# Performance work log

Hardware: AMD Instinct MI355X
Metric: run time of the kernel (lower is better)

Reference implementation:

```python
import jax, jax.numpy as jnp
import numpy as np

N_NODES = 100000
NFEAT, NHID, NCLASS = 128, 64, 40
N_EDGES = 1600000


def setup_inputs() -> dict:
    key = jax.random.key(0)
    k1, k2, k3, k4, k5, k6 = jax.random.split(key, 6)
    x = jax.random.normal(k1, (N_NODES, NFEAT), dtype=jnp.float32)
    edge_index = jax.random.randint(k2, (2, N_EDGES), 0, N_NODES, dtype=jnp.int64)
    s1 = 1.0 / np.sqrt(NFEAT)
    s2 = 1.0 / np.sqrt(NHID)
    W1 = jax.random.uniform(k3, (NFEAT, NHID), jnp.float32, -s1, s1)
    b1 = jax.random.uniform(k4, (NHID,), jnp.float32, -s1, s1)
    W2 = jax.random.uniform(k5, (NHID, NCLASS), jnp.float32, -s2, s2)
    b2 = jax.random.uniform(k6, (NCLASS,), jnp.float32, -s2, s2)
    return {"x": x, "edge_index": edge_index, "W1": W1, "b1": b1, "W2": W2, "b2": b2}


def _gcn_conv(x, W, b, src, dst, n_nodes):
    # linear
    h = x @ W + b  # [N, out]
    # degree of source nodes (self-loops already included in src/dst)
    deg = jax.ops.segment_sum(jnp.ones_like(src, dtype=h.dtype), src, num_segments=n_nodes)
    dinv = deg ** -0.5  # deg >= 1 due to self-loops
    norm = dinv[src] * dinv[dst]  # [E]
    msg = norm[:, None] * h[src]  # gather + normalize, [E, out]
    return jax.ops.segment_sum(msg, dst, num_segments=n_nodes)  # scatter-add


def reference(x, edge_index, W1, b1, W2, b2):
    n = x.shape[0]
    loop = jnp.arange(n, dtype=edge_index.dtype)
    src = jnp.concatenate([edge_index[0], loop])
    dst = jnp.concatenate([edge_index[1], loop])
    h = _gcn_conv(x, W1, b1, src, dst, n)
    h = jax.nn.relu(h)
    # dropout is identity in eval mode
    h = _gcn_conv(h, W2, b2, src, dst, n)
    return jax.nn.log_softmax(h, axis=1)
```

## Files before the change

### kernel.cpp

```cpp
#include <hip/hip_runtime.h>
#include <math.h>

#define NFEAT 128
#define NHID 64
#define NCLASS 40
#define NCHUNK 64
#define RANGE 16384

typedef _Float16 half4_t __attribute__((ext_vector_type(4)));
typedef _Float16 half8_t __attribute__((ext_vector_type(8)));
typedef float f32x4 __attribute__((ext_vector_type(4)));

__global__ __launch_bounds__(1024) void histdeg_kernel(
    const int* __restrict__ src, const int* __restrict__ dst, int E, int n,
    int nrange, unsigned short* __restrict__ deg_p,
    unsigned short* __restrict__ hist_p) {
    __shared__ unsigned int degc[RANGE / 2];
    __shared__ unsigned int histc[RANGE / 2];
    int c = blockIdx.x / nrange;
    int r = blockIdx.x - c * nrange;
    int r0 = r * RANGE;
    for (int i = threadIdx.x; i < RANGE / 2; i += 1024) {
        degc[i] = 0u;
        histc[i] = 0u;
    }
    __syncthreads();
    int e0 = (int)((long long)E * c / NCHUNK);
    int e1 = (int)((long long)E * (c + 1) / NCHUNK);
    for (int e = e0 + threadIdx.x * 4; e + 4 <= e1; e += 4096) {
        int4 s4 = *(const int4*)(src + e);
        int4 d4 = *(const int4*)(dst + e);
        int ss[4] = {s4.x, s4.y, s4.z, s4.w};
        int dd[4] = {d4.x, d4.y, d4.z, d4.w};
#pragma unroll
        for (int k = 0; k < 4; ++k) {
            int s = ss[k] - r0, d = dd[k] - r0;
            if ((unsigned)s < (unsigned)RANGE)
                atomicAdd(&degc[s >> 1], 1u << ((s & 1) * 16));
            if ((unsigned)d < (unsigned)RANGE)
                atomicAdd(&histc[d >> 1], 1u << ((d & 1) * 16));
        }
    }
    int tb = e0 + ((e1 - e0) & ~3);
    for (int e = tb + threadIdx.x; e < e1; e += 1024) {
        int s = src[e] - r0, d = dst[e] - r0;
        if ((unsigned)s < (unsigned)RANGE)
            atomicAdd(&degc[s >> 1], 1u << ((s & 1) * 16));
        if ((unsigned)d < (unsigned)RANGE)
            atomicAdd(&histc[d >> 1], 1u << ((d & 1) * 16));
    }
    __syncthreads();
    int hi = n - r0; if (hi > RANGE) hi = RANGE;
    for (int i = threadIdx.x; i < hi; i += 1024) {
        unsigned dv = (degc[i >> 1] >> ((i & 1) * 16)) & 0xFFFFu;
        unsigned hv = (histc[i >> 1] >> ((i & 1) * 16)) & 0xFFFFu;
        deg_p[(size_t)c * n + r0 + i] = (unsigned short)dv;
        hist_p[(size_t)c * n + r0 + i] = (unsigned short)hv;
    }
}

__global__ void reduce_kernel(const unsigned short* __restrict__ deg_p,
                              const unsigned short* __restrict__ hist_p,
                              float* __restrict__ dinv,
                              int* __restrict__ htot, int n) {
    int i = blockIdx.x * blockDim.x + threadIdx.x;
    if (i >= n) return;
    int d = 1, h = 0;
#pragma unroll 8
    for (int c = 0; c < NCHUNK; ++c) {
        d += deg_p[(size_t)c * n + i];
        h += hist_p[(size_t)c * n + i];
    }
    dinv[i] = rsqrtf((float)d);
    htot[i] = h;
}

__global__ void scan_block_kernel(const int* __restrict__ hist,
                                  int* __restrict__ scanned,
                                  int* __restrict__ bsums, int n) {
    __shared__ int tmp[256];
    int i = blockIdx.x * 256 + threadIdx.x;
    int v = (i < n) ? hist[i] : 0;
    tmp[threadIdx.x] = v;
    __syncthreads();
#pragma unroll
    for (int off = 1; off < 256; off <<= 1) {
        int t = (threadIdx.x >= off) ? tmp[threadIdx.x - off] : 0;
        __syncthreads();
        tmp[threadIdx.x] += t;
        __syncthreads();
    }
    if (i < n) scanned[i] = tmp[threadIdx.x] - v;
    if (threadIdx.x == 255) bsums[blockIdx.x] = tmp[255];
}

__global__ void scan_partials_kernel(int* __restrict__ bsums, int nb) {
    __shared__ int tmp[512];
    int v = (threadIdx.x < nb) ? bsums[threadIdx.x] : 0;
    tmp[threadIdx.x] = v;
    __syncthreads();
#pragma unroll
    for (int off = 1; off < 512; off <<= 1) {
        int t = (threadIdx.x >= off) ? tmp[threadIdx.x - off] : 0;
        __syncthreads();
        tmp[threadIdx.x] += t;
        __syncthreads();
    }
    if (threadIdx.x < nb) bsums[threadIdx.x] = tmp[threadIdx.x] - v;
}

__global__ void scan_add_kernel(const int* __restrict__ scanned,
                                const int* __restrict__ bsums,
                                int* __restrict__ row_start, int n, int E) {
    int i = blockIdx.x * 256 + threadIdx.x;
    if (i < n) row_start[i] = scanned[i] + bsums[blockIdx.x];
    if (i == 0) row_start[n] = E;
}

__global__ void base_kernel(const int* __restrict__ row_start,
                            const unsigned short* __restrict__ hist_p,
                            int* __restrict__ bases, int n) {
    int i = blockIdx.x * blockDim.x + threadIdx.x;
    if (i >= n) return;
    int r = row_start[i];
#pragma unroll 8
    for (int c = 0; c < NCHUNK; ++c) {
        bases[(size_t)c * n + i] = r;
        r += hist_p[(size_t)c * n + i];
    }
}

__global__ __launch_bounds__(1024) void scatter_kernel(
    const int* __restrict__ src, const int* __restrict__ dst, int E, int n,
    int nrange, const int* __restrict__ bases, int* __restrict__ es) {
    __shared__ int cur[RANGE];
    int c = blockIdx.x / nrange;
    int r = blockIdx.x - c * nrange;
    int r0 = r * RANGE;
    int hi = n - r0; if (hi > RANGE) hi = RANGE;
    for (int i = threadIdx.x; i < hi; i += 1024)
        cur[i] = bases[(size_t)c * n + r0 + i];
    __syncthreads();
    int e0 = (int)((long long)E * c / NCHUNK);
    int e1 = (int)((long long)E * (c + 1) / NCHUNK);
    for (int e = e0 + threadIdx.x * 4; e + 4 <= e1; e += 4096) {
        int4 s4 = *(const int4*)(src + e);
        int4 d4 = *(const int4*)(dst + e);
        int ss[4] = {s4.x, s4.y, s4.z, s4.w};
        int dd[4] = {d4.x, d4.y, d4.z, d4.w};
#pragma unroll
        for (int k = 0; k < 4; ++k) {
            int d = dd[k] - r0;
            if ((unsigned)d < (unsigned)hi) {
                int pos = atomicAdd(&cur[d], 1);
                es[pos] = ss[k];
            }
        }
    }
    int tb = e0 + ((e1 - e0) & ~3);
    for (int e = tb + threadIdx.x; e < e1; e += 1024) {
        int d = dst[e] - r0;
        if ((unsigned)d < (unsigned)hi) {
            int pos = atomicAdd(&cur[d], 1);
            es[pos] = src[e];
        }
    }
}

__global__ __launch_bounds__(256) void gemm1_mfma_kernel(
    const float* __restrict__ x, const float* __restrict__ W1,
    const float* __restrict__ b1, const float* __restrict__ dinv,
    _Float16* __restrict__ H1, int n) {
    int wave = threadIdx.x >> 6;
    int lane = threadIdx.x & 63;
    int lr = lane & 15;
    int kg = lane >> 4;
    half8_t bf[4][4];
    float b1v[4];
#pragma unroll
    for (int t = 0; t < 4; ++t) {
        int col = t * 16 + lr;
        b1v[t] = b1[col];
#pragma unroll
        for (int ks = 0; ks < 4; ++ks) {
            int kb = ks * 32 + kg * 8;
            half8_t hb;
#pragma unroll
            for (int j = 0; j < 8; ++j) hb[j] = (_Float16)W1[(kb + j) * NHID + col];
            bf[ks][t] = hb;
        }
    }
    int nt16 = (n + 15) >> 4;
    for (int gt = blockIdx.x * 4 + wave; gt < nt16; gt += gridDim.x * 4) {
        int m0 = gt * 16;
        int arow = m0 + lr; if (arow >= n) arow = n - 1;
        f32x4 acc[4] = {f32x4{0,0,0,0}, f32x4{0,0,0,0}, f32x4{0,0,0,0}, f32x4{0,0,0,0}};
#pragma unroll
        for (int ks = 0; ks < 4; ++ks) {
            const float* ap = x + (size_t)arow * NFEAT + ks * 32 + kg * 8;
            float4 a0 = *(const float4*)ap;
            float4 a1 = *(const float4*)(ap + 4);
            half8_t af;
            af[0] = (_Float16)a0.x; af[1] = (_Float16)a0.y;
            af[2] = (_Float16)a0.z; af[3] = (_Float16)a0.w;
            af[4] = (_Float16)a1.x; af[5] = (_Float16)a1.y;
            af[6] = (_Float16)a1.z; af[7] = (_Float16)a1.w;
#pragma unroll
            for (int t = 0; t < 4; ++t)
                acc[t] = __builtin_amdgcn_mfma_f32_16x16x32_f16(af, bf[ks][t], acc[t], 0, 0, 0);
        }
        int r0 = m0 + kg * 4;
        float dv[4];
#pragma unroll
        for (int r = 0; r < 4; ++r) {
            int rr = r0 + r;
            dv[r] = (rr < n) ? dinv[rr] : 0.f;
        }
#pragma unroll
        for (int t = 0; t < 4; ++t)
#pragma unroll
            for (int r = 0; r < 4; ++r) {
                int rr = r0 + r;
                if (rr < n)
                    H1[(size_t)rr * NHID + t * 16 + lr] =
                        (_Float16)((acc[t][r] + b1v[t]) * dv[r]);
            }
    }
}

__global__ __launch_bounds__(256) void agg1_kernel(
    const int* __restrict__ es, const int* __restrict__ row_start,
    const float* __restrict__ dinv, const _Float16* __restrict__ H1,
    _Float16* __restrict__ AGG, int n) {
    int wave = threadIdx.x >> 6;
    int lane = threadIdx.x & 63;
    int q = lane >> 4;
    int m = lane & 15;
    int stride = gridDim.x * 4;
    for (int node = blockIdx.x * 4 + wave; node < n; node += stride) {
        int e0 = row_start[node], e1 = row_start[node + 1];
        float a0 = 0.f, a1 = 0.f, a2 = 0.f, a3 = 0.f;
        for (int e = e0; e < e1; e += 64) {
            int cnt = e1 - e; if (cnt > 64) cnt = 64;
            int myE = es[e + ((lane < cnt) ? lane : 0)];
            for (int j = 0; j < cnt; j += 16) {
#pragma unroll
                for (int p = 0; p < 4; ++p) {
                    int jj = j + 4 * p + q;
                    int rr = __shfl(myE, jj, 64);
                    if (jj < cnt) {
                        half4_t v = *(const half4_t*)(H1 + (size_t)rr * NHID + 4 * m);
                        a0 += (float)v[0]; a1 += (float)v[1];
                        a2 += (float)v[2]; a3 += (float)v[3];
                    }
                }
            }
        }
        if (q == 0) {
            half4_t v = *(const half4_t*)(H1 + (size_t)node * NHID + 4 * m);
            a0 += (float)v[0]; a1 += (float)v[1];
            a2 += (float)v[2]; a3 += (float)v[3];
        }
        a0 += __shfl_xor(a0, 16, 64); a0 += __shfl_xor(a0, 32, 64);
        a1 += __shfl_xor(a1, 16, 64); a1 += __shfl_xor(a1, 32, 64);
        a2 += __shfl_xor(a2, 16, 64); a2 += __shfl_xor(a2, 32, 64);
        a3 += __shfl_xor(a3, 16, 64); a3 += __shfl_xor(a3, 32, 64);
        float di = dinv[node];
        if (lane < 16) {
            half4_t o;
            o[0] = (_Float16)fmaxf(a0 * di, 0.f);
            o[1] = (_Float16)fmaxf(a1 * di, 0.f);
            o[2] = (_Float16)fmaxf(a2 * di, 0.f);
            o[3] = (_Float16)fmaxf(a3 * di, 0.f);
            *(half4_t*)(AGG + (size_t)node * NHID + 4 * lane) = o;
        }
    }
}

__global__ __launch_bounds__(256) void gemm2_mfma_kernel(
    const _Float16* __restrict__ AGG, const float* __restrict__ W2,
    const float* __restrict__ b2, const float* __restrict__ dinv,
    _Float16* __restrict__ H2, int n) {
    int wave = threadIdx.x >> 6;
    int lane = threadIdx.x & 63;
    int lr = lane & 15;
    int kg = lane >> 4;
    half8_t bf[2][3];
    float b2v[3];
#pragma unroll
    for (int t = 0; t < 3; ++t) {
        int col = t * 16 + lr;
        b2v[t] = (col < NCLASS) ? b2[col] : 0.f;
#pragma unroll
        for (int ks = 0; ks < 2; ++ks) {
            int kb = ks * 32 + kg * 8;
            half8_t hb;
#pragma unroll
            for (int j = 0; j < 8; ++j)
                hb[j] = (col < NCLASS) ? (_Float16)W2[(kb + j) * NCLASS + col]
                                       : (_Float16)0.f;
            bf[ks][t] = hb;
        }
    }
    int nt16 = (n + 15) >> 4;
    for (int gt = blockIdx.x * 4 + wave; gt < nt16; gt += gridDim.x * 4) {
        int m0 = gt * 16;
        int arow = m0 + lr; if (arow >= n) arow = n - 1;
        f32x4 acc[3] = {f32x4{0,0,0,0}, f32x4{0,0,0,0}, f32x4{0,0,0,0}};
#pragma unroll
        for (int ks = 0; ks < 2; ++ks) {
            half8_t af = *(const half8_t*)(AGG + (size_t)arow * NHID + ks * 32 + kg * 8);
#pragma unroll
            for (int t = 0; t < 3; ++t)
                acc[t] = __builtin_amdgcn_mfma_f32_16x16x32_f16(af, bf[ks][t], acc[t], 0, 0, 0);
        }
        int r0 = m0 + kg * 4;
        float dv[4];
#pragma unroll
        for (int r = 0; r < 4; ++r) {
            int rr = r0 + r;
            dv[r] = (rr < n) ? dinv[rr] : 0.f;
        }
#pragma unroll
        for (int t = 0; t < 3; ++t) {
            int col = t * 16 + lr;
#pragma unroll
            for (int r = 0; r < 4; ++r) {
                int rr = r0 + r;
                if (rr < n)
                    H2[(size_t)rr * 64 + col] =
                        (col < NCLASS) ? (_Float16)((acc[t][r] + b2v[t]) * dv[r])
                                       : (_Float16)0.f;
            }
        }
    }
}

__global__ __launch_bounds__(256) void agg2_lsm_kernel(
    const int* __restrict__ es, const int* __restrict__ row_start,
    const float* __restrict__ dinv, const _Float16* __restrict__ H2,
    float* __restrict__ out, int n) {
    int wave = threadIdx.x >> 6;
    int lane = threadIdx.x & 63;
    int q = lane >> 4;
    int m = lane & 15;
    int stride = gridDim.x * 4;
    for (int node = blockIdx.x * 4 + wave; node < n; node += stride) {
        int e0 = row_start[node], e1 = row_start[node + 1];
        float a0 = 0.f, a1 = 0.f, a2 = 0.f, a3 = 0.f;
        for (int e = e0; e < e1; e += 64) {
            int cnt = e1 - e; if (cnt > 64) cnt = 64;
            int myE = es[e + ((lane < cnt) ? lane : 0)];
            for (int j = 0; j < cnt; j += 16) {
#pragma unroll
                for (int p = 0; p < 4; ++p) {
                    int jj = j + 4 * p + q;
                    int rr = __shfl(myE, jj, 64);
                    if (jj < cnt) {
                        half4_t v = *(const half4_t*)(H2 + (size_t)rr * 64 + 4 * m);
                        a0 += (float)v[0]; a1 += (float)v[1];
                        a2 += (float)v[2]; a3 += (float)v[3];
                    }
                }
            }
        }
        if (q == 0) {
            half4_t v = *(const half4_t*)(H2 + (size_t)node * 64 + 4 * m);
            a0 += (float)v[0]; a1 += (float)v[1];
            a2 += (float)v[2]; a3 += (float)v[3];
        }
        a0 += __shfl_xor(a0, 16, 64); a0 += __shfl_xor(a0, 32, 64);
        a1 += __shfl_xor(a1, 16, 64); a1 += __shfl_xor(a1, 32, 64);
        a2 += __shfl_xor(a2, 16, 64); a2 += __shfl_xor(a2, 32, 64);
        a3 += __shfl_xor(a3, 16, 64); a3 += __shfl_xor(a3, 32, 64);
        float di = dinv[node];
        float v0 = a0 * di, v1 = a1 * di, v2 = a2 * di, v3 = a3 * di;
        bool valid = (m < 10);
        float vmax = valid ? fmaxf(fmaxf(v0, v1), fmaxf(v2, v3)) : -INFINITY;
#pragma unroll
        for (int off = 8; off; off >>= 1) vmax = fmaxf(vmax, __shfl_xor(vmax, off, 64));
        float sume = valid ? (__expf(v0 - vmax) + __expf(v1 - vmax) +
                              __expf(v2 - vmax) + __expf(v3 - vmax)) : 0.f;
#pragma unroll
        for (int off = 8; off; off >>= 1) sume += __shfl_xor(sume, off, 64);
        float lse = __logf(sume) + vmax;
        if (lane < 10) {
            float4 o = make_float4(v0 - lse, v1 - lse, v2 - lse, v3 - lse);
            *(float4*)(out + (size_t)node * NCLASS + 4 * lane) = o;
        }
    }
}

extern "C" void kernel_launch(void* const* d_in, const int* in_sizes, int n_in,
                              void* d_out, int out_size, void* d_ws, size_t ws_size,
                              hipStream_t stream) {
    const float* x  = (const float*)d_in[0];
    const int*   ei = (const int*)d_in[1];
    const float* W1 = (const float*)d_in[2];
    const float* b1 = (const float*)d_in[3];
    const float* W2 = (const float*)d_in[4];
    const float* b2 = (const float*)d_in[5];
    float* out = (float*)d_out;

    const int n = in_sizes[0] / NFEAT;
    const int E = in_sizes[1] / 2;
    const int* src = ei;
    const int* dst = ei + E;
    const int nrange = (n + RANGE - 1) / RANGE;

    char* ws = (char*)d_ws;
    float*          dinv      = (float*)(ws + 0);
    int*            htot      = (int*)(ws + (512 << 10));
    int*            scanned   = (int*)(ws + (1024 << 10));
    int*            row_start = (int*)(ws + (1536 << 10));
    int*            bsums     = (int*)(ws + (2048 << 10));
    unsigned short* deg_p     = (unsigned short*)(ws + (3u << 20));
    unsigned short* hist_p    = (unsigned short*)(ws + (16u << 20));
    int*            bases     = (int*)(ws + (29u << 20));
    int*            es        = (int*)(ws + (3u << 20));
    _Float16*       H2        = (_Float16*)(ws + (16u << 20));
    _Float16*       H1        = (_Float16*)(ws + (29u << 20));
    _Float16*       AGG       = (_Float16*)(ws + (42u << 20));

    const int blk = 256;
    const int nblk_n = (n + blk - 1) / blk;
    const int gridbin = NCHUNK * nrange;

    histdeg_kernel<<<gridbin, 1024, 0, stream>>>(src, dst, E, n, nrange, deg_p, hist_p);
    reduce_kernel<<<nblk_n, blk, 0, stream>>>(deg_p, hist_p, dinv, htot, n);

    scan_block_kernel<<<nblk_n, blk, 0, stream>>>(htot, scanned, bsums, n);
    scan_partials_kernel<<<1, 512, 0, stream>>>(bsums, nblk_n);
    scan_add_kernel<<<nblk_n, blk, 0, stream>>>(scanned, bsums, row_start, n, E);
    base_kernel<<<nblk_n, blk, 0, stream>>>(row_start, hist_p, bases, n);

    scatter_kernel<<<gridbin, 1024, 0, stream>>>(src, dst, E, n, nrange, bases, es);

    gemm1_mfma_kernel<<<512, blk, 0, stream>>>(x, W1, b1, dinv, H1, n);

    agg1_kernel<<<4096, blk, 0, stream>>>(es, row_start, dinv, H1, AGG, n);

    gemm2_mfma_kernel<<<512, blk, 0, stream>>>(AGG, W2, b2, dinv, H2, n);

    agg2_lsm_kernel<<<4096, blk, 0, stream>>>(es, row_start, dinv, H2, out, n);
}
```

Before: 309.9 us.

## Widen histogram range, compact H2 to 40 columns, use 32-bit index math

The histogram kernel now covers 32768 nodes per block, which halves the number of passes over the edge list. The scatter kernel keeps its 16384-node range. H2 is now stored with a 40-column stride instead of a padded 64, and agg2 masks out the lanes that held padding, so each gathered row moves less data. Index arithmetic in the aggregation kernels switches from 64-bit multiplies to 32-bit shifts. The larger histogram range doubles LDS use (128KB), which could lower occupancy or fail to launch if it exceeds the LDS limit.

```diff
diff --git a/kernel.cpp b/kernel.cpp
--- a/kernel.cpp
+++ b/kernel.cpp
@@ -5,7 +5,8 @@
 #define NHID 64
 #define NCLASS 40
 #define NCHUNK 64
-#define RANGE 16384
+#define RANGE_H 32768
+#define RANGE_S 16384
 
 typedef _Float16 half4_t __attribute__((ext_vector_type(4)));
 typedef _Float16 half8_t __attribute__((ext_vector_type(8)));
@@ -15,12 +16,12 @@
     const int* __restrict__ src, const int* __restrict__ dst, int E, int n,
     int nrange, unsigned short* __restrict__ deg_p,
     unsigned short* __restrict__ hist_p) {
-    __shared__ unsigned int degc[RANGE / 2];
-    __shared__ unsigned int histc[RANGE / 2];
+    __shared__ unsigned int degc[RANGE_H / 2];
+    __shared__ unsigned int histc[RANGE_H / 2];
     int c = blockIdx.x / nrange;
     int r = blockIdx.x - c * nrange;
-    int r0 = r * RANGE;
-    for (int i = threadIdx.x; i < RANGE / 2; i += 1024) {
+    int r0 = r * RANGE_H;
+    for (int i = threadIdx.x; i < RANGE_H / 2; i += 1024) {
         degc[i] = 0u;
         histc[i] = 0u;
     }
@@ -35,22 +36,22 @@
 #pragma unroll
         for (int k = 0; k < 4; ++k) {
             int s = ss[k] - r0, d = dd[k] - r0;
-            if ((unsigned)s < (unsigned)RANGE)
+            if ((unsigned)s < (unsigned)RANGE_H)
                 atomicAdd(&degc[s >> 1], 1u << ((s & 1) * 16));
-            if ((unsigned)d < (unsigned)RANGE)
+            if ((unsigned)d < (unsigned)RANGE_H)
                 atomicAdd(&histc[d >> 1], 1u << ((d & 1) * 16));
         }
     }
     int tb = e0 + ((e1 - e0) & ~3);
     for (int e = tb + threadIdx.x; e < e1; e += 1024) {
         int s = src[e] - r0, d = dst[e] - r0;
-        if ((unsigned)s < (unsigned)RANGE)
+        if ((unsigned)s < (unsigned)RANGE_H)
             atomicAdd(&degc[s >> 1], 1u << ((s & 1) * 16));
-        if ((unsigned)d < (unsigned)RANGE)
+        if ((unsigned)d < (unsigned)RANGE_H)
             atomicAdd(&histc[d >> 1], 1u << ((d & 1) * 16));
     }
     __syncthreads();
-    int hi = n - r0; if (hi > RANGE) hi = RANGE;
+    int hi = n - r0; if (hi > RANGE_H) hi = RANGE_H;
     for (int i = threadIdx.x; i < hi; i += 1024) {
         unsigned dv = (degc[i >> 1] >> ((i & 1) * 16)) & 0xFFFFu;
         unsigned hv = (histc[i >> 1] >> ((i & 1) * 16)) & 0xFFFFu;
@@ -133,11 +134,11 @@
 __global__ __launch_bounds__(1024) void scatter_kernel(
     const int* __restrict__ src, const int* __restrict__ dst, int E, int n,
     int nrange, const int* __restrict__ bases, int* __restrict__ es) {
-    __shared__ int cur[RANGE];
+    __shared__ int cur[RANGE_S];
     int c = blockIdx.x / nrange;
     int r = blockIdx.x - c * nrange;
-    int r0 = r * RANGE;
-    int hi = n - r0; if (hi > RANGE) hi = RANGE;
+    int r0 = r * RANGE_S;
+    int hi = n - r0; if (hi > RANGE_S) hi = RANGE_S;
     for (int i = threadIdx.x; i < hi; i += 1024)
         cur[i] = bases[(size_t)c * n + r0 + i];
     __syncthreads();
@@ -249,7 +250,8 @@
                     int jj = j + 4 * p + q;
                     int rr = __shfl(myE, jj, 64);
                     if (jj < cnt) {
-                        half4_t v = *(const half4_t*)(H1 + (size_t)rr * NHID + 4 * m);
+                        int off = (rr << 6) + (m << 2);
+                        half4_t v = *(const half4_t*)(H1 + off);
                         a0 += (float)v[0]; a1 += (float)v[1];
                         a2 += (float)v[2]; a3 += (float)v[3];
                     }
@@ -257,7 +259,7 @@
             }
         }
         if (q == 0) {
-            half4_t v = *(const half4_t*)(H1 + (size_t)node * NHID + 4 * m);
+            half4_t v = *(const half4_t*)(H1 + (node << 6) + (m << 2));
             a0 += (float)v[0]; a1 += (float)v[1];
             a2 += (float)v[2]; a3 += (float)v[3];
         }
@@ -272,7 +274,7 @@
             o[1] = (_Float16)fmaxf(a1 * di, 0.f);
             o[2] = (_Float16)fmaxf(a2 * di, 0.f);
             o[3] = (_Float16)fmaxf(a3 * di, 0.f);
-            *(half4_t*)(AGG + (size_t)node * NHID + 4 * lane) = o;
+            *(half4_t*)(AGG + (node << 6) + (lane << 2)) = o;
         }
     }
 }
@@ -309,7 +311,7 @@
         f32x4 acc[3] = {f32x4{0,0,0,0}, f32x4{0,0,0,0}, f32x4{0,0,0,0}};
 #pragma unroll
         for (int ks = 0; ks < 2; ++ks) {
-            half8_t af = *(const half8_t*)(AGG + (size_t)arow * NHID + ks * 32 + kg * 8);
+            half8_t af = *(const half8_t*)(AGG + ((size_t)arow << 6) + ks * 32 + kg * 8);
 #pragma unroll
             for (int t = 0; t < 3; ++t)
                 acc[t] = __builtin_amdgcn_mfma_f32_16x16x32_f16(af, bf[ks][t], acc[t], 0, 0, 0);
@@ -324,13 +326,14 @@
 #pragma unroll
         for (int t = 0; t < 3; ++t) {
             int col = t * 16 + lr;
-#pragma unroll
-            for (int r = 0; r < 4; ++r) {
-                int rr = r0 + r;
-                if (rr < n)
-                    H2[(size_t)rr * 64 + col] =
-                        (col < NCLASS) ? (_Float16)((acc[t][r] + b2v[t]) * dv[r])
-                                       : (_Float16)0.f;
+            if (col < NCLASS) {
+#pragma unroll
+                for (int r = 0; r < 4; ++r) {
+                    int rr = r0 + r;
+                    if (rr < n)
+                        H2[(size_t)rr * NCLASS + col] =
+                            (_Float16)((acc[t][r] + b2v[t]) * dv[r]);
+                }
             }
         }
     }
@@ -344,6 +347,7 @@
     int lane = threadIdx.x & 63;
     int q = lane >> 4;
     int m = lane & 15;
+    bool valid = (m < 10);
     int stride = gridDim.x * 4;
     for (int node = blockIdx.x * 4 + wave; node < n; node += stride) {
         int e0 = row_start[node], e1 = row_start[node + 1];
@@ -356,16 +360,18 @@
                 for (int p = 0; p < 4; ++p) {
                     int jj = j + 4 * p + q;
                     int rr = __shfl(myE, jj, 64);
-                    if (jj < cnt) {
-                        half4_t v = *(const half4_t*)(H2 + (size_t)rr * 64 + 4 * m);
+                    if (valid && jj < cnt) {
+                        int off = (((rr << 2) + rr) << 3) + (m << 2);
+                        half4_t v = *(const half4_t*)(H2 + off);
                         a0 += (float)v[0]; a1 += (float)v[1];
                         a2 += (float)v[2]; a3 += (float)v[3];
                     }
                 }
             }
         }
-        if (q == 0) {
-            half4_t v = *(const half4_t*)(H2 + (size_t)node * 64 + 4 * m);
+        if (q == 0 && valid) {
+            int off = (((node << 2) + node) << 3) + (m << 2);
+            half4_t v = *(const half4_t*)(H2 + off);
             a0 += (float)v[0]; a1 += (float)v[1];
             a2 += (float)v[2]; a3 += (float)v[3];
         }
@@ -375,7 +381,6 @@
         a3 += __shfl_xor(a3, 16, 64); a3 += __shfl_xor(a3, 32, 64);
         float di = dinv[node];
         float v0 = a0 * di, v1 = a1 * di, v2 = a2 * di, v3 = a3 * di;
-        bool valid = (m < 10);
         float vmax = valid ? fmaxf(fmaxf(v0, v1), fmaxf(v2, v3)) : -INFINITY;
 #pragma unroll
         for (int off = 8; off; off >>= 1) vmax = fmaxf(vmax, __shfl_xor(vmax, off, 64));
@@ -406,7 +411,8 @@
     const int E = in_sizes[1] / 2;
     const int* src = ei;
     const int* dst = ei + E;
-    const int nrange = (n + RANGE - 1) / RANGE;
+    const int nrange_h = (n + RANGE_H - 1) / RANGE_H;
+    const int nrange_s = (n + RANGE_S - 1) / RANGE_S;
 
     char* ws = (char*)d_ws;
     float*          dinv      = (float*)(ws + 0);
@@ -424,9 +430,9 @@
 
     const int blk = 256;
     const int nblk_n = (n + blk - 1) / blk;
-    const int gridbin = NCHUNK * nrange;
-
-    histdeg_kernel<<<gridbin, 1024, 0, stream>>>(src, dst, E, n, nrange, deg_p, hist_p);
+
+    histdeg_kernel<<<NCHUNK * nrange_h, 1024, 0, stream>>>(src, dst, E, n, nrange_h,
+                                                           deg_p, hist_p);
     reduce_kernel<<<nblk_n, blk, 0, stream>>>(deg_p, hist_p, dinv, htot, n);
 
     scan_block_kernel<<<nblk_n, blk, 0, stream>>>(htot, scanned, bsums, n);
@@ -434,7 +440,8 @@
     scan_add_kernel<<<nblk_n, blk, 0, stream>>>(scanned, bsums, row_start, n, E);
     base_kernel<<<nblk_n, blk, 0, stream>>>(row_start, hist_p, bases, n);
 
-    scatter_kernel<<<gridbin, 1024, 0, stream>>>(src, dst, E, n, nrange, bases, es);
+    scatter_kernel<<<NCHUNK * nrange_s, 1024, 0, stream>>>(src, dst, E, n, nrange_s,
+                                                           bases, es);
 
     gemm1_mfma_kernel<<<512, blk, 0, stream>>>(x, W1, b1, dinv, H1, n);
 
```

New measurement: 306.4 us. Within noise of the previous version (-1.1%).
